# Performance work log

Hardware: AMD Instinct MI355X
Metric: run time of the kernel (lower is better)

The kernel has to match this reference:

```python
import jax, jax.numpy as jnp
import numpy as np

N_NODES = 50000
N_EDGES = 800000
N_GRAPHS = 512
NODE_DIM, EDGE_DIM, HID, OUT = 96, 16, 128, 128


def _gine_conv(x, src, dst, edge_attr, We, be, W1, b1, W2, b2, eps=0.0):
    # messages: ReLU(x_j + Lin_edge(edge_attr)), gathered at source nodes
    msg = jax.nn.relu(x[src] + edge_attr @ We + be)          # [E, d]
    agg = jax.ops.segment_sum(msg, dst, num_segments=N_NODES)  # [N, d]
    h = (1.0 + eps) * x + agg
    # GIN MLP: Linear -> ReLU -> Linear
    return jax.nn.relu(h @ W1 + b1) @ W2 + b2


def setup_inputs() -> dict:
    key = jax.random.key(0)
    ks = jax.random.split(key, 16)
    x = jax.random.normal(ks[0], (N_NODES, NODE_DIM), jnp.float32)
    edge_index = jax.random.randint(ks[1], (2, N_EDGES), 0, N_NODES, jnp.int32)
    edge_attr = jax.random.normal(ks[2], (N_EDGES, EDGE_DIM), jnp.float32)
    batch = jnp.sort(jax.random.randint(ks[3], (N_NODES,), 0, N_GRAPHS, jnp.int32))

    def lin(k, fi, fo):
        s = 1.0 / np.sqrt(fi)
        kw, kb = jax.random.split(k)
        return (jax.random.uniform(kw, (fi, fo), jnp.float32, -s, s),
                jax.random.uniform(kb, (fo,), jnp.float32, -s, s))

    We1, be1 = lin(ks[4], EDGE_DIM, NODE_DIM)
    W1a, b1a = lin(ks[5], NODE_DIM, HID)
    W1b, b1b = lin(ks[6], HID, HID)
    We2, be2 = lin(ks[7], EDGE_DIM, HID)
    W2a, b2a = lin(ks[8], HID, HID)
    W2b, b2b = lin(ks[9], HID, HID)
    Wfc, bfc = lin(ks[10], HID, OUT)
    return {"x": x, "edge_index": edge_index, "edge_attr": edge_attr, "batch": batch,
            "We1": We1, "be1": be1, "W1a": W1a, "b1a": b1a, "W1b": W1b, "b1b": b1b,
            "We2": We2, "be2": be2, "W2a": W2a, "b2a": b2a, "W2b": W2b, "b2b": b2b,
            "Wfc": Wfc, "bfc": bfc}


def reference(x, edge_index, edge_attr, batch,
              We1, be1, W1a, b1a, W1b, b1b,
              We2, be2, W2a, b2a, W2b, b2b,
              Wfc, bfc):
    src, dst = edge_index[0], edge_index[1]
    h = jax.nn.relu(_gine_conv(x, src, dst, edge_attr, We1, be1, W1a, b1a, W1b, b1b))
    h = jax.nn.relu(_gine_conv(h, src, dst, edge_attr, We2, be2, W2a, b2a, W2b, b2b))
    pooled = jax.ops.segment_sum(h, batch, num_segments=N_GRAPHS)  # [G, HID]
    return pooled @ Wfc + bfc
```

## Files before the change

kernel.cpp:

```cpp
#include <hip/hip_runtime.h>
#include <hip/hip_bf16.h>

#define N_NODES 50000
#define N_EDGES 800000
#define N_GRAPHS 512

typedef __attribute__((ext_vector_type(8))) short short8v;
typedef __attribute__((ext_vector_type(4))) float f32x4;

__device__ inline float bf2f(unsigned short u) {
    union { unsigned int i; float f; } v; v.i = ((unsigned int)u) << 16; return v.f;
}
__device__ inline short f2bf(float f) {
    __hip_bfloat16 h = __float2bfloat16(f);
    return *reinterpret_cast<short*>(&h);
}


__global__ __launch_bounds__(256) void count_deg(
    const int* __restrict__ dst, int* __restrict__ deg)
{
    int e = blockIdx.x * blockDim.x + threadIdx.x;
    if (e < N_EDGES) atomicAdd(&deg[dst[e]], 1);
}

__global__ __launch_bounds__(256) void assign_base(
    const int* __restrict__ deg, int* __restrict__ basep, int* __restrict__ counter)
{
    int n = blockIdx.x * blockDim.x + threadIdx.x;
    if (n < N_NODES) basep[n] = atomicAdd(counter, deg[n]);
}

__global__ __launch_bounds__(256) void scatter_edges(
    const int* __restrict__ dst, const int* __restrict__ src,
    const float* __restrict__ ea,
    const int* __restrict__ basep, int* __restrict__ fill,
    unsigned short* __restrict__ srcdst, unsigned short* __restrict__ eadst)
{
    int e = blockIdx.x * blockDim.x + threadIdx.x;
    if (e < N_EDGES) {
        const int d = dst[e];
        const int slot = atomicAdd(&fill[d], 1);
        const size_t pos = (size_t)basep[d] + slot;
        srcdst[pos] = (unsigned short)src[e];
        const float4* ap = (const float4*)(ea + (size_t)e * 16);
        const float4 a0 = ap[0], a1 = ap[1], a2 = ap[2], a3 = ap[3];
        short8v o0, o1;
        o0[0] = f2bf(a0.x); o0[1] = f2bf(a0.y); o0[2] = f2bf(a0.z); o0[3] = f2bf(a0.w);
        o0[4] = f2bf(a1.x); o0[5] = f2bf(a1.y); o0[6] = f2bf(a1.z); o0[7] = f2bf(a1.w);
        o1[0] = f2bf(a2.x); o1[1] = f2bf(a2.y); o1[2] = f2bf(a2.z); o1[3] = f2bf(a2.w);
        o1[4] = f2bf(a3.x); o1[5] = f2bf(a3.y); o1[6] = f2bf(a3.z); o1[7] = f2bf(a3.w);
        ((short8v*)eadst)[2 * pos]     = o0;
        ((short8v*)eadst)[2 * pos + 1] = o1;
    }
}

#define T0_CVT (N_NODES * 48)
__global__ __launch_bounds__(256) void prep_convert(
    const float* __restrict__ x,
    const float* __restrict__ W1a, const float* __restrict__ W1b,
    const float* __restrict__ W2a, const float* __restrict__ W2b,
    unsigned int* __restrict__ x16,
    unsigned short* __restrict__ W1aT, unsigned short* __restrict__ W1bT,
    unsigned short* __restrict__ W2aT, unsigned short* __restrict__ W2bT)
{
    int t = blockIdx.x * blockDim.x + threadIdx.x;
    if (t < T0_CVT) {
        const int m2 = t % 48;
        const int n  = t / 48;
        const int p  = m2 >> 4;
        const int c  = m2 & 15;
        const float lo = x[(size_t)n * 96 + 32 * p + c];
        const float hi = x[(size_t)n * 96 + 32 * p + 16 + c];
        x16[t] = (unsigned int)(unsigned short)f2bf(lo) |
                 ((unsigned int)(unsigned short)f2bf(hi) << 16);
        return;
    }
    int u = t - T0_CVT;
    if (u < 128 * 96) {
        W1aT[u] = (unsigned short)f2bf(W1a[(u % 96) * 128 + u / 96]);
        return;
    }
    u -= 128 * 96;
    if (u < 16384) { W1bT[u] = (unsigned short)f2bf(W1b[(u & 127) * 128 + (u >> 7)]); return; }
    u -= 16384;
    if (u < 16384) { W2aT[u] = (unsigned short)f2bf(W2a[(u & 127) * 128 + (u >> 7)]); return; }
    u -= 16384;
    if (u < 16384) { W2bT[u] = (unsigned short)f2bf(W2b[(u & 127) * 128 + (u >> 7)]); }
}

template <int DIN>
__global__ __launch_bounds__(256, 8) void gather_v8(
    const unsigned short* __restrict__ hin,
    const unsigned short* __restrict__ srcdst,
    const unsigned short* __restrict__ eadst,
    const int* __restrict__ deg,
    const int* __restrict__ basep,
    const float* __restrict__ We,
    const float* __restrict__ be,
    unsigned short* __restrict__ hpre)
{
    constexpr int NB = DIN / 16;
    constexpr int NP = DIN / 32;

    const int lane = threadIdx.x & 63;
    const int col = lane & 15;
    const int grp = lane >> 4;
    const int gwave = (blockIdx.x * blockDim.x + threadIdx.x) >> 6;
    const int nwaves = (gridDim.x * blockDim.x) >> 6;

    short8v Bf[NB];
#pragma unroll
    for (int b = 0; b < NB; ++b) {
        short8v f = {};
        if (grp < 2) {
#pragma unroll
            for (int j = 0; j < 8; ++j)
                f[j] = f2bf(We[(grp * 8 + j) * DIN + b * 16 + col]);
        } else if (grp == 2) {
            f[0] = f2bf(be[b * 16 + col]);
        }
        Bf[b] = f;
    }

    for (int n = gwave; n < N_NODES; n += nwaves) {
        const int dgc = deg[n];
        const int nch = (dgc + 15) >> 4;
        const int b0 = basep[n];

        float accv[NB];
#pragma unroll
        for (int b = 0; b < NB; ++b) accv[b] = 0.0f;

        for (int c = 0; c < nch; ++c) {
            const int pos0 = b0 + 16 * c;
            const int vcc = min(dgc - 16 * c, 16);

            int s_l = 0;
            if (lane < vcc) s_l = srcdst[pos0 + lane];

            short8v Af = {};
            if (grp < 2) {
                if (col < vcc)
                    Af = *(const short8v*)(eadst + (size_t)(pos0 + col) * 16 + grp * 8);
            } else if (grp == 2) {
                Af[0] = (short)0x3F80;
            }

            int sid[4];
#pragma unroll
            for (int r = 0; r < 4; ++r) sid[r] = __shfl(s_l, 4 * grp + r);

#pragma unroll
            for (int p = 0; p < NP; ++p) {
                const f32x4 zero = {0.0f, 0.0f, 0.0f, 0.0f};
                f32x4 lin0 = __builtin_amdgcn_mfma_f32_16x16x32_bf16(Af, Bf[2 * p], zero, 0, 0, 0);
                f32x4 lin1 = __builtin_amdgcn_mfma_f32_16x16x32_bf16(Af, Bf[2 * p + 1], zero, 0, 0, 0);
                float part0 = 0.0f, part1 = 0.0f;
#pragma unroll
                for (int r = 0; r < 4; ++r) {
                    if (4 * grp + r < vcc) {
                        const unsigned int u = *(const unsigned int*)
                            (hin + (size_t)sid[r] * DIN + 32 * p + 2 * col);
                        const float xlo = bf2f((unsigned short)(u & 0xffffu));
                        const float xhi = bf2f((unsigned short)(u >> 16));
                        part0 += fmaxf(xlo + lin0[r], 0.0f);
                        part1 += fmaxf(xhi + lin1[r], 0.0f);
                    }
                }
                accv[2 * p]     += part0;
                accv[2 * p + 1] += part1;
            }
        }

#pragma unroll
        for (int b = 0; b < NB; ++b) {
            accv[b] += __shfl_xor(accv[b], 16);
            accv[b] += __shfl_xor(accv[b], 32);
        }

        const float t0l = __shfl(accv[0], col), t0h = __shfl(accv[1], col);
        const float t1l = __shfl(accv[2], col), t1h = __shfl(accv[3], col);
        const float t2l = __shfl(accv[4], col), t2h = __shfl(accv[5], col);
        float lo, hi;
        if (DIN == 128) {
            const float t3l = __shfl(accv[NB - 2], col), t3h = __shfl(accv[NB - 1], col);
            lo = (grp == 0) ? t0l : (grp == 1) ? t1l : (grp == 2) ? t2l : t3l;
            hi = (grp == 0) ? t0h : (grp == 1) ? t1h : (grp == 2) ? t2h : t3h;
        } else {
            lo = (grp == 0) ? t0l : (grp == 1) ? t1l : t2l;
            hi = (grp == 0) ? t0h : (grp == 1) ? t1h : t2h;
        }

        if (lane < DIN / 2) {
            const unsigned int u =
                ((const unsigned int*)(hin + (size_t)n * DIN))[lane];
            const float slo = bf2f((unsigned short)(u & 0xffffu)) + lo;
            const float shi = bf2f((unsigned short)(u >> 16)) + hi;
            ((unsigned int*)(hpre + (size_t)n * DIN))[lane] =
                (unsigned int)(unsigned short)f2bf(slo) |
                ((unsigned int)(unsigned short)f2bf(shi) << 16);
        }
    }
}

template <int DIN, int MODE>
__global__ __launch_bounds__(256) void mlp_mfma(
    const unsigned short* __restrict__ hpre,
    const unsigned short* __restrict__ WaT,
    const float* __restrict__ ba,
    const unsigned short* __restrict__ WbT,
    const float* __restrict__ bb,
    unsigned short* __restrict__ h1out,
    const int* __restrict__ batch,
    float* __restrict__ pooled)
{
    constexpr int KS1 = DIN / 32;
    __shared__ unsigned short hls[32][DIN + 8];
    __shared__ unsigned short uls[32][128 + 8];
    __shared__ float vls[(MODE == 1) ? 32 : 1][(MODE == 1) ? 132 : 1];

    const int n0 = blockIdx.x * 32;
    const int tid = threadIdx.x;

    for (int f = tid * 4; f < 32 * DIN; f += 1024) {
        const int row = f / DIN, colc = f % DIN;
        const int n = n0 + row;
        ushort4 u = make_ushort4(0, 0, 0, 0);
        if (n < N_NODES) u = *(const ushort4*)(hpre + (size_t)n * DIN + colc);
        const int p = colc >> 5;
        const int q = (colc & 31) >> 2;
        hls[row][32 * p + 2 * q]          = u.x;
        hls[row][32 * p + 16 + 2 * q]     = u.y;
        hls[row][32 * p + 2 * q + 1]      = u.z;
        hls[row][32 * p + 16 + 2 * q + 1] = u.w;
    }
    __syncthreads();

    const int lane = tid & 63;
    const int w = tid >> 6;
    const int col = lane & 15;
    const int grp = lane >> 4;

    f32x4 acc00 = {0,0,0,0}, acc01 = {0,0,0,0}, acc10 = {0,0,0,0}, acc11 = {0,0,0,0};
#pragma unroll
    for (int ks = 0; ks < KS1; ++ks) {
        const short8v A0 = *(const short8v*)&hls[col][ks * 32 + grp * 8];
        const short8v A1 = *(const short8v*)&hls[16 + col][ks * 32 + grp * 8];
        const short8v B0 = *(const short8v*)&WaT[(size_t)(2 * w * 16 + col) * DIN + ks * 32 + grp * 8];
        const short8v B1 = *(const short8v*)&WaT[(size_t)((2 * w + 1) * 16 + col) * DIN + ks * 32 + grp * 8];
        acc00 = __builtin_amdgcn_mfma_f32_16x16x32_bf16(A0, B0, acc00, 0, 0, 0);
        acc01 = __builtin_amdgcn_mfma_f32_16x16x32_bf16(A0, B1, acc01, 0, 0, 0);
        acc10 = __builtin_amdgcn_mfma_f32_16x16x32_bf16(A1, B0, acc10, 0, 0, 0);
        acc11 = __builtin_amdgcn_mfma_f32_16x16x32_bf16(A1, B1, acc11, 0, 0, 0);
    }
    const float ba0 = ba[2 * w * 16 + col];
    const float ba1 = ba[(2 * w + 1) * 16 + col];
#pragma unroll
    for (int i = 0; i < 4; ++i) {
        const int r0 = grp * 4 + i;
        uls[r0][2 * w * 16 + col]            = (unsigned short)f2bf(fmaxf(acc00[i] + ba0, 0.f));
        uls[r0][(2 * w + 1) * 16 + col]      = (unsigned short)f2bf(fmaxf(acc01[i] + ba1, 0.f));
        uls[16 + r0][2 * w * 16 + col]       = (unsigned short)f2bf(fmaxf(acc10[i] + ba0, 0.f));
        uls[16 + r0][(2 * w + 1) * 16 + col] = (unsigned short)f2bf(fmaxf(acc11[i] + ba1, 0.f));
    }
    __syncthreads();

    acc00 = (f32x4){0,0,0,0}; acc01 = (f32x4){0,0,0,0};
    acc10 = (f32x4){0,0,0,0}; acc11 = (f32x4){0,0,0,0};
#pragma unroll
    for (int ks = 0; ks < 4; ++ks) {
        const short8v A0 = *(const short8v*)&uls[col][ks * 32 + grp * 8];
        const short8v A1 = *(const short8v*)&uls[16 + col][ks * 32 + grp * 8];
        const short8v B0 = *(const short8v*)&WbT[(size_t)(2 * w * 16 + col) * 128 + ks * 32 + grp * 8];
        const short8v B1 = *(const short8v*)&WbT[(size_t)((2 * w + 1) * 16 + col) * 128 + ks * 32 + grp * 8];
        acc00 = __builtin_amdgcn_mfma_f32_16x16x32_bf16(A0, B0, acc00, 0, 0, 0);
        acc01 = __builtin_amdgcn_mfma_f32_16x16x32_bf16(A0, B1, acc01, 0, 0, 0);
        acc10 = __builtin_amdgcn_mfma_f32_16x16x32_bf16(A1, B0, acc10, 0, 0, 0);
        acc11 = __builtin_amdgcn_mfma_f32_16x16x32_bf16(A1, B1, acc11, 0, 0, 0);
    }
    const float bb0 = bb[2 * w * 16 + col];
    const float bb1 = bb[(2 * w + 1) * 16 + col];

    if (MODE == 0) {
#pragma unroll
        for (int i = 0; i < 4; ++i) {
            const int nA = n0 + grp * 4 + i;
            if (nA < N_NODES) {
                const float v0 = fmaxf(acc00[i] + bb0, 0.f);
                const float v1 = fmaxf(acc01[i] + bb1, 0.f);
                *(unsigned int*)(h1out + (size_t)nA * 128 + 32 * w + 2 * col) =
                    (unsigned int)(unsigned short)f2bf(v0) |
                    ((unsigned int)(unsigned short)f2bf(v1) << 16);
            }
            const int nB = n0 + 16 + grp * 4 + i;
            if (nB < N_NODES) {
                const float v0 = fmaxf(acc10[i] + bb0, 0.f);
                const float v1 = fmaxf(acc11[i] + bb1, 0.f);
                *(unsigned int*)(h1out + (size_t)nB * 128 + 32 * w + 2 * col) =
                    (unsigned int)(unsigned short)f2bf(v0) |
                    ((unsigned int)(unsigned short)f2bf(v1) << 16);
            }
        }
    } else {
#pragma unroll
        for (int i = 0; i < 4; ++i) {
            const int r0 = grp * 4 + i;
            vls[r0][2 * w * 16 + col]            = fmaxf(acc00[i] + bb0, 0.f);
            vls[r0][(2 * w + 1) * 16 + col]      = fmaxf(acc01[i] + bb1, 0.f);
            vls[16 + r0][2 * w * 16 + col]       = fmaxf(acc10[i] + bb0, 0.f);
            vls[16 + r0][(2 * w + 1) * 16 + col] = fmaxf(acc11[i] + bb1, 0.f);
        }
        __syncthreads();
        if (tid < 128) {
            const int d = tid;
            const int lim = min(32, N_NODES - n0);
            float s = 0.0f;
            int bprev = -1;
            for (int q = 0; q < lim; ++q) {
                const int b = batch[n0 + q];
                if (b != bprev) {
                    if (bprev >= 0) atomicAdd(&pooled[bprev * 128 + d], s);
                    s = 0.0f;
                    bprev = b;
                }
                s += vls[q][d];
            }
            if (bprev >= 0) atomicAdd(&pooled[bprev * 128 + d], s);
        }
    }
}

__global__ __launch_bounds__(128) void fc_kernel(
    const float* __restrict__ pooled,
    const float* __restrict__ Wfc,
    const float* __restrict__ bfc,
    float* __restrict__ out)
{
    const int g = blockIdx.x;
    const int d = threadIdx.x;
    __shared__ float sp[128];
    sp[d] = pooled[g * 128 + d];
    __syncthreads();
    float acc = bfc[d];
    for (int k = 0; k < 128; ++k) acc = fmaf(sp[k], Wfc[k * 128 + d], acc);
    out[g * 128 + d] = acc;
}

extern "C" void kernel_launch(void* const* d_in, const int* in_sizes, int n_in,
                              void* d_out, int out_size, void* d_ws, size_t ws_size,
                              hipStream_t stream) {
    const float* x    = (const float*)d_in[0];
    const int*   eidx = (const int*)d_in[1];
    const float* ea   = (const float*)d_in[2];
    const int*   batch= (const int*)d_in[3];
    const float* We1  = (const float*)d_in[4];
    const float* be1  = (const float*)d_in[5];
    const float* W1a  = (const float*)d_in[6];
    const float* b1a  = (const float*)d_in[7];
    const float* W1b  = (const float*)d_in[8];
    const float* b1b  = (const float*)d_in[9];
    const float* We2  = (const float*)d_in[10];
    const float* be2  = (const float*)d_in[11];
    const float* W2a  = (const float*)d_in[12];
    const float* b2a  = (const float*)d_in[13];
    const float* W2b  = (const float*)d_in[14];
    const float* b2b  = (const float*)d_in[15];
    const float* Wfc  = (const float*)d_in[16];
    const float* bfc  = (const float*)d_in[17];
    float* out = (float*)d_out;

    const int* srcp = eidx;
    const int* dstp = eidx + N_EDGES;

    const int gblocks = 2048;
    const int mblocks = (N_NODES + 31) / 32;

    char* w = (char*)d_ws;
    unsigned short* bufA = (unsigned short*)w;  w += (size_t)N_NODES * 128 * 2;
    unsigned short* bufB = (unsigned short*)w;  w += (size_t)N_NODES * 128 * 2;
    int* deg   = (int*)w;                       w += (size_t)N_NODES * 4;
    int* basep = (int*)w;                       w += (size_t)N_NODES * 4;
    int* fillp = (int*)w;                       w += (size_t)N_NODES * 4;
    int* counter = (int*)w;                     w += 256;
    unsigned short* srcdst = (unsigned short*)w; w += (size_t)N_EDGES * 2;
    unsigned short* eadst = (unsigned short*)w;  w += (size_t)N_EDGES * 16 * 2;
    float* pooled = (float*)w;                  w += (size_t)N_GRAPHS * 128 * 4;
    unsigned short* W1aT = (unsigned short*)w;  w += (size_t)128 * 96 * 2;
    unsigned short* W1bT = (unsigned short*)w;  w += (size_t)128 * 128 * 2;
    unsigned short* W2aT = (unsigned short*)w;  w += (size_t)128 * 128 * 2;
    unsigned short* W2bT = (unsigned short*)w;  w += (size_t)128 * 128 * 2;

    unsigned short* x16 = bufB;

    hipMemsetAsync(deg, 0, (size_t)N_NODES * 4, stream);
    hipMemsetAsync(fillp, 0, (size_t)N_NODES * 4, stream);
    hipMemsetAsync(counter, 0, 4, stream);
    count_deg<<<(N_EDGES + 255) / 256, 256, 0, stream>>>(dstp, deg);
    assign_base<<<(N_NODES + 255) / 256, 256, 0, stream>>>(deg, basep, counter);
    scatter_edges<<<(N_EDGES + 255) / 256, 256, 0, stream>>>(
        dstp, srcp, ea, basep, fillp, srcdst, eadst);
    {
        const int total = T0_CVT + 128 * 96 + 3 * 16384;
        prep_convert<<<(total + 255) / 256, 256, 0, stream>>>(
            x, W1a, W1b, W2a, W2b, (unsigned int*)x16, W1aT, W1bT, W2aT, W2bT);
    }

    gather_v8<96><<<gblocks, 256, 0, stream>>>(
        x16, srcdst, eadst, deg, basep, We1, be1, bufA);
    mlp_mfma<96, 0><<<mblocks, 256, 0, stream>>>(
        bufA, W1aT, b1a, W1bT, b1b, bufB, nullptr, nullptr);

    gather_v8<128><<<gblocks, 256, 0, stream>>>(
        bufB, srcdst, eadst, deg, basep, We2, be2, bufA);
    hipMemsetAsync(pooled, 0, (size_t)N_GRAPHS * 128 * 4, stream);
    mlp_mfma<128, 1><<<mblocks, 256, 0, stream>>>(
        bufA, W2aT, b2a, W2bT, b2b, nullptr, batch, pooled);

    fc_kernel<<<N_GRAPHS, 128, 0, stream>>>(pooled, Wfc, bfc, out);
}
```

Measured before the change: 369.4 us.

## Prefetch next edge chunk in gather, contiguous node ranges, fold memsets into kernels

The gather kernel now gives each wave a contiguous range of nodes instead of a strided loop. It prefetches the next node's degree and base, loads the self row early, and software-pipelines the next chunk's source indices and edge attributes. The memsets of deg, fill and counter move into the prep_convert kernel, and the pooled buffer is zeroed inside the second gather kernel, which removes separate memset launches. The epilogue is simplified to shuffle the self row and write from 16 lanes. In exchange, the contiguous node split can unbalance work across waves and the prefetch raises register pressure.

Measured after the change: 433.8 us. 17.4% more time.

```diff
diff --git a/kernel.cpp b/kernel.cpp
--- a/kernel.cpp
+++ b/kernel.cpp
@@ -56,13 +56,15 @@
 }
 
 #define T0_CVT (N_NODES * 48)
+#define TW_CVT (128 * 96 + 3 * 16384)
 __global__ __launch_bounds__(256) void prep_convert(
     const float* __restrict__ x,
     const float* __restrict__ W1a, const float* __restrict__ W1b,
     const float* __restrict__ W2a, const float* __restrict__ W2b,
     unsigned int* __restrict__ x16,
     unsigned short* __restrict__ W1aT, unsigned short* __restrict__ W1bT,
-    unsigned short* __restrict__ W2aT, unsigned short* __restrict__ W2bT)
+    unsigned short* __restrict__ W2aT, unsigned short* __restrict__ W2bT,
+    int* __restrict__ deg, int* __restrict__ fillp, int* __restrict__ counter)
 {
     int t = blockIdx.x * blockDim.x + threadIdx.x;
     if (t < T0_CVT) {
@@ -77,20 +79,23 @@
         return;
     }
     int u = t - T0_CVT;
-    if (u < 128 * 96) {
-        W1aT[u] = (unsigned short)f2bf(W1a[(u % 96) * 128 + u / 96]);
-        return;
-    }
+    if (u < 128 * 96) { W1aT[u] = (unsigned short)f2bf(W1a[(u % 96) * 128 + u / 96]); return; }
     u -= 128 * 96;
     if (u < 16384) { W1bT[u] = (unsigned short)f2bf(W1b[(u & 127) * 128 + (u >> 7)]); return; }
     u -= 16384;
     if (u < 16384) { W2aT[u] = (unsigned short)f2bf(W2a[(u & 127) * 128 + (u >> 7)]); return; }
     u -= 16384;
-    if (u < 16384) { W2bT[u] = (unsigned short)f2bf(W2b[(u & 127) * 128 + (u >> 7)]); }
+    if (u < 16384) { W2bT[u] = (unsigned short)f2bf(W2b[(u & 127) * 128 + (u >> 7)]); return; }
+    u -= 16384;
+    if (u < N_NODES) { deg[u] = 0; return; }
+    u -= N_NODES;
+    if (u < N_NODES) { fillp[u] = 0; return; }
+    u -= N_NODES;
+    if (u == 0) { *counter = 0; }
 }
 
 template <int DIN>
-__global__ __launch_bounds__(256, 8) void gather_v8(
+__global__ __launch_bounds__(256, 8) void gather_v9(
     const unsigned short* __restrict__ hin,
     const unsigned short* __restrict__ srcdst,
     const unsigned short* __restrict__ eadst,
@@ -98,10 +103,18 @@
     const int* __restrict__ basep,
     const float* __restrict__ We,
     const float* __restrict__ be,
-    unsigned short* __restrict__ hpre)
+    unsigned short* __restrict__ hpre,
+    float* __restrict__ pooled_zero)
 {
     constexpr int NB = DIN / 16;
     constexpr int NP = DIN / 32;
+
+    if (pooled_zero) {
+        const int t = blockIdx.x * blockDim.x + threadIdx.x;
+        if (t < N_GRAPHS * 128 / 4) {
+            ((float4*)pooled_zero)[t] = make_float4(0.f, 0.f, 0.f, 0.f);
+        }
+    }
 
     const int lane = threadIdx.x & 63;
     const int col = lane & 15;
@@ -123,39 +136,69 @@
         Bf[b] = f;
     }
 
-    for (int n = gwave; n < N_NODES; n += nwaves) {
-        const int dgc = deg[n];
+    const int K = (N_NODES + nwaves - 1) / nwaves;
+    const int n_beg = gwave * K;
+    if (n_beg >= N_NODES) return;
+    const int n_end = min(n_beg + K, N_NODES);
+
+    int dg_n = deg[n_beg];
+    int bp_n = basep[n_beg];
+
+    for (int n = n_beg; n < n_end; ++n) {
+        int dg_nx = 0, bp_nx = 0;
+        if (n + 1 < n_end) { dg_nx = deg[n + 1]; bp_nx = basep[n + 1]; }
+
+        unsigned int selfu = 0;
+        if (lane < DIN / 2)
+            selfu = ((const unsigned int*)(hin + (size_t)n * DIN))[lane];
+
+        const int dgc = dg_n;
+        const int b0  = bp_n;
         const int nch = (dgc + 15) >> 4;
-        const int b0 = basep[n];
 
         float accv[NB];
 #pragma unroll
         for (int b = 0; b < NB; ++b) accv[b] = 0.0f;
 
+        int s_cur = 0;
+        short8v ea_cur = {};
+        if (nch > 0) {
+            const int vcc0 = min(dgc, 16);
+            if (lane < vcc0) s_cur = srcdst[b0 + lane];
+            if (grp < 2) {
+                if (col < vcc0)
+                    ea_cur = *(const short8v*)(eadst + (size_t)(b0 + col) * 16 + grp * 8);
+            } else if (grp == 2) {
+                ea_cur[0] = (short)0x3F80;
+            }
+        }
+
         for (int c = 0; c < nch; ++c) {
-            const int pos0 = b0 + 16 * c;
             const int vcc = min(dgc - 16 * c, 16);
 
-            int s_l = 0;
-            if (lane < vcc) s_l = srcdst[pos0 + lane];
-
-            short8v Af = {};
-            if (grp < 2) {
-                if (col < vcc)
-                    Af = *(const short8v*)(eadst + (size_t)(pos0 + col) * 16 + grp * 8);
-            } else if (grp == 2) {
-                Af[0] = (short)0x3F80;
+            int s_nxt = 0;
+            short8v ea_nxt = {};
+            if (c + 1 < nch) {
+                const int vccn = min(dgc - 16 * (c + 1), 16);
+                const int posn = b0 + 16 * (c + 1);
+                if (lane < vccn) s_nxt = srcdst[posn + lane];
+                if (grp < 2) {
+                    if (col < vccn)
+                        ea_nxt = *(const short8v*)(eadst + (size_t)(posn + col) * 16 + grp * 8);
+                } else if (grp == 2) {
+                    ea_nxt[0] = (short)0x3F80;
+                }
             }
 
             int sid[4];
 #pragma unroll
-            for (int r = 0; r < 4; ++r) sid[r] = __shfl(s_l, 4 * grp + r);
+            for (int r = 0; r < 4; ++r) sid[r] = __shfl(s_cur, 4 * grp + r);
 
 #pragma unroll
             for (int p = 0; p < NP; ++p) {
                 const f32x4 zero = {0.0f, 0.0f, 0.0f, 0.0f};
-                f32x4 lin0 = __builtin_amdgcn_mfma_f32_16x16x32_bf16(Af, Bf[2 * p], zero, 0, 0, 0);
-                f32x4 lin1 = __builtin_amdgcn_mfma_f32_16x16x32_bf16(Af, Bf[2 * p + 1], zero, 0, 0, 0);
+                f32x4 lin0 = __builtin_amdgcn_mfma_f32_16x16x32_bf16(ea_cur, Bf[2 * p], zero, 0, 0, 0);
+                f32x4 lin1 = __builtin_amdgcn_mfma_f32_16x16x32_bf16(ea_cur, Bf[2 * p + 1], zero, 0, 0, 0);
                 float part0 = 0.0f, part1 = 0.0f;
 #pragma unroll
                 for (int r = 0; r < 4; ++r) {
@@ -171,6 +214,9 @@
                 accv[2 * p]     += part0;
                 accv[2 * p + 1] += part1;
             }
+
+            s_cur = s_nxt;
+            ea_cur = ea_nxt;
         }
 
 #pragma unroll
@@ -179,28 +225,24 @@
             accv[b] += __shfl_xor(accv[b], 32);
         }
 
-        const float t0l = __shfl(accv[0], col), t0h = __shfl(accv[1], col);
-        const float t1l = __shfl(accv[2], col), t1h = __shfl(accv[3], col);
-        const float t2l = __shfl(accv[4], col), t2h = __shfl(accv[5], col);
-        float lo, hi;
-        if (DIN == 128) {
-            const float t3l = __shfl(accv[NB - 2], col), t3h = __shfl(accv[NB - 1], col);
-            lo = (grp == 0) ? t0l : (grp == 1) ? t1l : (grp == 2) ? t2l : t3l;
-            hi = (grp == 0) ? t0h : (grp == 1) ? t1h : (grp == 2) ? t2h : t3h;
-        } else {
-            lo = (grp == 0) ? t0l : (grp == 1) ? t1l : t2l;
-            hi = (grp == 0) ? t0h : (grp == 1) ? t1h : t2h;
-        }
-
-        if (lane < DIN / 2) {
-            const unsigned int u =
-                ((const unsigned int*)(hin + (size_t)n * DIN))[lane];
-            const float slo = bf2f((unsigned short)(u & 0xffffu)) + lo;
-            const float shi = bf2f((unsigned short)(u >> 16)) + hi;
-            ((unsigned int*)(hpre + (size_t)n * DIN))[lane] =
-                (unsigned int)(unsigned short)f2bf(slo) |
-                ((unsigned int)(unsigned short)f2bf(shi) << 16);
-        }
+        unsigned int up[NP];
+#pragma unroll
+        for (int p = 0; p < NP; ++p)
+            up[p] = __shfl(selfu, 16 * p + (lane & 15));
+
+        if (lane < 16) {
+#pragma unroll
+            for (int p = 0; p < NP; ++p) {
+                const float lo = bf2f((unsigned short)(up[p] & 0xffffu)) + accv[2 * p];
+                const float hi = bf2f((unsigned short)(up[p] >> 16)) + accv[2 * p + 1];
+                *(unsigned int*)(hpre + (size_t)n * DIN + 32 * p + 2 * lane) =
+                    (unsigned int)(unsigned short)f2bf(lo) |
+                    ((unsigned int)(unsigned short)f2bf(hi) << 16);
+            }
+        }
+
+        dg_n = dg_nx;
+        bp_n = bp_nx;
     }
 }
 
@@ -393,27 +435,24 @@
 
     unsigned short* x16 = bufB;
 
-    hipMemsetAsync(deg, 0, (size_t)N_NODES * 4, stream);
-    hipMemsetAsync(fillp, 0, (size_t)N_NODES * 4, stream);
-    hipMemsetAsync(counter, 0, 4, stream);
+    {
+        const int total = T0_CVT + TW_CVT + 2 * N_NODES + 1;
+        prep_convert<<<(total + 255) / 256, 256, 0, stream>>>(
+            x, W1a, W1b, W2a, W2b, (unsigned int*)x16,
+            W1aT, W1bT, W2aT, W2bT, deg, fillp, counter);
+    }
     count_deg<<<(N_EDGES + 255) / 256, 256, 0, stream>>>(dstp, deg);
     assign_base<<<(N_NODES + 255) / 256, 256, 0, stream>>>(deg, basep, counter);
     scatter_edges<<<(N_EDGES + 255) / 256, 256, 0, stream>>>(
         dstp, srcp, ea, basep, fillp, srcdst, eadst);
-    {
-        const int total = T0_CVT + 128 * 96 + 3 * 16384;
-        prep_convert<<<(total + 255) / 256, 256, 0, stream>>>(
-            x, W1a, W1b, W2a, W2b, (unsigned int*)x16, W1aT, W1bT, W2aT, W2bT);
-    }
-
-    gather_v8<96><<<gblocks, 256, 0, stream>>>(
-        x16, srcdst, eadst, deg, basep, We1, be1, bufA);
+
+    gather_v9<96><<<gblocks, 256, 0, stream>>>(
+        x16, srcdst, eadst, deg, basep, We1, be1, bufA, nullptr);
     mlp_mfma<96, 0><<<mblocks, 256, 0, stream>>>(
         bufA, W1aT, b1a, W1bT, b1b, bufB, nullptr, nullptr);
 
-    gather_v8<128><<<gblocks, 256, 0, stream>>>(
-        bufB, srcdst, eadst, deg, basep, We2, be2, bufA);
-    hipMemsetAsync(pooled, 0, (size_t)N_GRAPHS * 128 * 4, stream);
+    gather_v9<128><<<gblocks, 256, 0, stream>>>(
+        bufB, srcdst, eadst, deg, basep, We2, be2, bufA, pooled);
     mlp_mfma<128, 1><<<mblocks, 256, 0, stream>>>(
         bufA, W2aT, b2a, W2bT, b2b, nullptr, batch, pooled);
 
```
